# Optimization experiments

Hardware: AMD Instinct MI355X
Metric: run time of the kernel (lower is better)

Reference implementation:

```python
import jax, jax.numpy as jnp
import numpy as np

N_NODES = 50000
N_EDGES = 800000
N_GRAPHS = 256
IN_DIM = 128
HID = 512            # hidden_layer_size
H2 = HID // 2        # 256, conv channels
H4 = HID // 4        # 128


def _linear_init(key, fan_in, fan_out):
    kw, kb = jax.random.split(key)
    bound = 1.0 / np.sqrt(fan_in)
    W = jax.random.uniform(kw, (fan_in, fan_out), minval=-bound, maxval=bound, dtype=jnp.float32)
    b = jax.random.uniform(kb, (fan_out,), minval=-bound, maxval=bound, dtype=jnp.float32)
    return W, b


def setup_inputs() -> dict:
    key = jax.random.key(0)
    ks = jax.random.split(key, 8)
    x = jax.random.normal(ks[0], (N_NODES, IN_DIM), dtype=jnp.float32)
    edge_index = jax.random.randint(ks[1], (2, N_EDGES), 0, N_NODES, dtype=jnp.int64)
    batch = jnp.sort(jax.random.randint(ks[2], (N_NODES,), 0, N_GRAPHS, dtype=jnp.int64))
    W1, b1 = _linear_init(ks[3], IN_DIM, HID)
    Wc1, bc1 = _linear_init(ks[4], HID, H2)
    Wc2, bc2 = _linear_init(ks[5], H2, H2)
    W2, b2 = _linear_init(ks[6], H2, H4)
    W3, b3 = _linear_init(ks[7], H4, 1)
    return {"x": x, "edge_index": edge_index, "batch": batch,
            "W1": W1, "b1": b1, "Wc1": Wc1, "bc1": bc1,
            "Wc2": Wc2, "bc2": bc2, "W2": W2, "b2": b2, "W3": W3, "b3": b3}


def _gcn_conv(h, W, b, src, dst, norm):
    # PyG GCNConv: out = scatter_add(norm * (h @ W)[src] -> dst) + b
    hw = h @ W                                   # [N, C_out]
    msg = norm[:, None] * hw[src]                # [E+N, C_out] gather
    agg = jax.ops.segment_sum(msg, dst, num_segments=N_NODES)  # scatter-add
    return agg + b


def reference(x, edge_index, batch, W1, b1, Wc1, bc1, Wc2, bc2, W2, b2, W3, b3):
    # --- symmetric GCN normalization with self-loops (shared by both convs) ---
    loop = jnp.arange(N_NODES, dtype=edge_index.dtype)
    src = jnp.concatenate([edge_index[0], loop])
    dst = jnp.concatenate([edge_index[1], loop])
    deg = jax.ops.segment_sum(jnp.ones_like(dst, dtype=jnp.float32), dst, num_segments=N_NODES)
    dinv = jax.lax.rsqrt(deg)                    # deg >= 1 thanks to self-loops
    norm = dinv[src] * dinv[dst]                 # [E+N]

    h = jax.nn.relu(x @ W1 + b1)                 # lin1
    h = jax.nn.relu(_gcn_conv(h, Wc1, bc1, src, dst, norm))   # conv1
    h = jax.nn.relu(_gcn_conv(h, Wc2, bc2, src, dst, norm))   # conv2

    # global_mean_pool over graph ids
    sums = jax.ops.segment_sum(h, batch, num_segments=N_GRAPHS)
    counts = jax.ops.segment_sum(jnp.ones((N_NODES,), jnp.float32), batch, num_segments=N_GRAPHS)
    g = sums / jnp.maximum(counts, 1.0)[:, None]

    # F.dropout is identity in deterministic/eval reference
    g = jax.nn.relu(g @ W2 + b2)                 # lin2
    return g @ W3 + b3                           # lin3 -> [N_GRAPHS, 1]
```

## Files before the change

kernel.cpp:

```cpp
#include <hip/hip_runtime.h>
#include <hip/hip_bf16.h>

#define NN 50000
#define NE 800000
#define NG 256
#define DIN 128
#define DH 512
#define DC 256
#define DL 128
#define NB 49

#define XBF_OFF   0UL
#define H1BF_OFF  12800000UL
#define HWBF_OFF  64000000UL
#define H2BF_OFF  89600000UL
#define H3BF_OFF  115200000UL
#define W1T_OFF   140800000UL
#define WC1T_OFF  140931072UL
#define WC2T_OFF  141193216UL
#define CNT_OFF   141324288UL
#define FILL_OFF  141524288UL
#define DINV_OFF  141724288UL
#define RP_OFF    141924288UL
#define BSUM_OFF  142124416UL
#define EW_OFF    142124800UL

using bf16x8 = __attribute__((ext_vector_type(8))) short;
using u16x8  = __attribute__((ext_vector_type(8))) unsigned short;
using f32x4  = __attribute__((ext_vector_type(4))) float;

__device__ __forceinline__ short f2bf(float f) {
  unsigned u = __builtin_bit_cast(unsigned, f);
  unsigned r = u + 0x7fffu + ((u >> 16) & 1u);
  return (short)(r >> 16);
}
__device__ __forceinline__ float bf2f(unsigned short u) {
  return __builtin_bit_cast(float, (unsigned)u << 16);
}

__device__ __forceinline__ void gload_lds16(const void* g, void* l) {
  typedef const __attribute__((address_space(1))) unsigned gu32;
  typedef __attribute__((address_space(3))) unsigned lu32;
  __builtin_amdgcn_global_load_lds((gu32*)g, (lu32*)l, 16, 0, 0);
}

__global__ void count_in(const int* __restrict__ dst, int* __restrict__ cnt) {
  int e = blockIdx.x * blockDim.x + threadIdx.x;
  if (e < NE) atomicAdd(&cnt[dst[e]], 1);
}

__global__ __launch_bounds__(1024) void scan_p1(const int* __restrict__ cnt,
                                                int* __restrict__ rowptr,
                                                int* __restrict__ bsum,
                                                float* __restrict__ dinv) {
  __shared__ int wsum[16];
  const int idx = blockIdx.x * 1024 + threadIdx.x;
  const int lane = threadIdx.x & 63, wid = threadIdx.x >> 6;
  int v = (idx < NN) ? cnt[idx] : 0;
  int incl = v;
  #pragma unroll
  for (int s = 1; s < 64; s <<= 1) {
    int t = __shfl_up(incl, s, 64);
    if (lane >= s) incl += t;
  }
  if (lane == 63) wsum[wid] = incl;
  __syncthreads();
  if (wid == 0 && lane < 16) {
    int w = wsum[lane];
    int wincl = w;
    #pragma unroll
    for (int s = 1; s < 16; s <<= 1) {
      int t = __shfl_up(wincl, s, 64);
      if (lane >= s) wincl += t;
    }
    wsum[lane] = wincl - w;
    if (lane == 15) bsum[blockIdx.x] = wincl;
  }
  __syncthreads();
  if (idx < NN) {
    rowptr[idx] = wsum[wid] + incl - v;
    dinv[idx] = 1.0f / sqrtf((float)(v + 1));
  }
}

__global__ void scan_p2(int* __restrict__ bsum, int* __restrict__ rowptr) {
  const int lane = threadIdx.x;
  int v = (lane < NB) ? bsum[lane] : 0;
  int incl = v;
  #pragma unroll
  for (int s = 1; s < 64; s <<= 1) {
    int t = __shfl_up(incl, s, 64);
    if (lane >= s) incl += t;
  }
  if (lane < NB) bsum[lane] = incl - v;
  if (lane == 63) rowptr[NN] = incl;
}

__global__ __launch_bounds__(1024) void scan_p3(int* __restrict__ rowptr,
                                                const int* __restrict__ bsum) {
  const int idx = blockIdx.x * 1024 + threadIdx.x;
  if (idx < NN && blockIdx.x > 0) rowptr[idx] += bsum[blockIdx.x];
}

__global__ void fill_csr(const int* __restrict__ src, const int* __restrict__ dst,
                         const int* __restrict__ rowptr, int* __restrict__ fill,
                         const float* __restrict__ dinv, int2* __restrict__ ew) {
  int e = blockIdx.x * blockDim.x + threadIdx.x;
  if (e < NE) {
    int d = dst[e];
    int s = src[e];
    int pos = rowptr[d] + atomicAdd(&fill[d], 1);
    ew[pos] = make_int2(s, __float_as_int(dinv[d] * dinv[s]));
  }
}

__global__ void cvt_bf16(const float* __restrict__ in, short* __restrict__ out, int n8) {
  int i = blockIdx.x * blockDim.x + threadIdx.x;
  if (i >= n8) return;
  const float4* p = (const float4*)in + (long)i * 2;
  float4 a = p[0], b = p[1];
  bf16x8 o;
  o[0] = f2bf(a.x); o[1] = f2bf(a.y); o[2] = f2bf(a.z); o[3] = f2bf(a.w);
  o[4] = f2bf(b.x); o[5] = f2bf(b.y); o[6] = f2bf(b.z); o[7] = f2bf(b.w);
  *(bf16x8*)(out + (long)i * 8) = o;
}

__global__ void transpose_bf16(const float* __restrict__ in, short* __restrict__ out,
                               int K, int N) {
  int idx = blockIdx.x * blockDim.x + threadIdx.x;
  if (idx >= K * N) return;
  int n = idx / K, k = idx % K;
  out[idx] = f2bf(in[k * N + n]);
}

template<int DO_RELU, int HAS_BIAS>
__global__ __launch_bounds__(256) void gemm_mfma2(
    const short* __restrict__ A,
    const short* __restrict__ Bt,
    const float* __restrict__ bias,
    short* __restrict__ Cout, int M, int K, int N)
{
  __shared__ __align__(16) short As[128][32];
  __shared__ __align__(16) short Bs[128][32];
  const int tid  = threadIdx.x;
  const int lane = tid & 63;
  const int wave = tid >> 6;
  const int wr   = wave >> 1;
  const int wc   = wave & 1;
  const int bm = blockIdx.y * 128;
  const int bn = blockIdx.x * 128;

  const int srow = lane >> 2;
  const int scol = (lane & 3) * 8;

  f32x4 acc[4][4];
  #pragma unroll
  for (int m = 0; m < 4; ++m)
    #pragma unroll
    for (int n = 0; n < 4; ++n)
      acc[m][n] = f32x4{0.f, 0.f, 0.f, 0.f};

  const int fr = lane & 15;
  const int kb = (lane >> 4) * 8;

  for (int k0 = 0; k0 < K; k0 += 32) {
    #pragma unroll
    for (int j = 0; j < 2; ++j) {
      const int r = wave * 32 + j * 16;
      gload_lds16(A  + (long)(bm + r + srow) * K + k0 + scol, &As[r][0]);
      gload_lds16(Bt + (long)(bn + r + srow) * K + k0 + scol, &Bs[r][0]);
    }
    __syncthreads();
    bf16x8 af[4], bfr[4];
    #pragma unroll
    for (int m = 0; m < 4; ++m)
      af[m] = *(const bf16x8*)&As[wr * 64 + m * 16 + fr][kb];
    #pragma unroll
    for (int n = 0; n < 4; ++n)
      bfr[n] = *(const bf16x8*)&Bs[wc * 64 + n * 16 + fr][kb];
    #pragma unroll
    for (int m = 0; m < 4; ++m)
      #pragma unroll
      for (int n = 0; n < 4; ++n)
        acc[m][n] = __builtin_amdgcn_mfma_f32_16x16x32_bf16(af[m], bfr[n], acc[m][n], 0, 0, 0);
    __syncthreads();
  }

  const int cr4 = (lane >> 4) * 4;
  const int cc  = lane & 15;
  #pragma unroll
  for (int m = 0; m < 4; ++m) {
    #pragma unroll
    for (int r = 0; r < 4; ++r) {
      int gm = bm + wr * 64 + m * 16 + cr4 + r;
      if (gm >= M) continue;
      #pragma unroll
      for (int n = 0; n < 4; ++n) {
        int gn = bn + wc * 64 + n * 16 + cc;
        float v = acc[m][n][r];
        if (HAS_BIAS) v += bias[gn];
        if (DO_RELU) v = fmaxf(v, 0.f);
        Cout[(long)gm * N + gn] = f2bf(v);
      }
    }
  }
}

__global__ __launch_bounds__(256) void aggregate_v4(
    const unsigned short* __restrict__ hw, const int2* __restrict__ ew,
    const int* __restrict__ rowptr, const float* __restrict__ dinv,
    const float* __restrict__ bias, unsigned short* __restrict__ out)
{
  const int wid  = threadIdx.x >> 6;
  const int lane = threadIdx.x & 63;
  const int i = blockIdx.x * 4 + wid;
  if (i >= NN) return;
  const int half = lane >> 5;
  const int c0 = (lane & 31) * 8;

  float acc[8] = {0.f, 0.f, 0.f, 0.f, 0.f, 0.f, 0.f, 0.f};
  if (half == 0) {
    const float di = dinv[i];
    const float w = di * di;
    u16x8 sv = *(const u16x8*)(hw + (long)i * DC + c0);
    #pragma unroll
    for (int k = 0; k < 8; ++k) acc[k] = w * bf2f(sv[k]);
  }

  const int s0 = rowptr[i], s1 = rowptr[i + 1];
  int e = s0;
  for (; e + 16 <= s1; e += 16) {
    int nn[8]; float wv[8]; u16x8 vv[8];
    #pragma unroll
    for (int j = 0; j < 8; ++j) {
      int2 p = ew[e + 2 * j + half];
      nn[j] = p.x; wv[j] = __int_as_float(p.y);
    }
    #pragma unroll
    for (int j = 0; j < 8; ++j)
      vv[j] = *(const u16x8*)(hw + (long)nn[j] * DC + c0);
    #pragma unroll
    for (int j = 0; j < 8; ++j)
      #pragma unroll
      for (int k = 0; k < 8; ++k) acc[k] += wv[j] * bf2f(vv[j][k]);
  }
  for (; e + 2 <= s1; e += 2) {
    int2 p = ew[e + half];
    u16x8 v = *(const u16x8*)(hw + (long)p.x * DC + c0);
    float w = __int_as_float(p.y);
    #pragma unroll
    for (int k = 0; k < 8; ++k) acc[k] += w * bf2f(v[k]);
  }
  if (e < s1 && half == 0) {
    int2 p = ew[e];
    u16x8 v = *(const u16x8*)(hw + (long)p.x * DC + c0);
    float w = __int_as_float(p.y);
    #pragma unroll
    for (int k = 0; k < 8; ++k) acc[k] += w * bf2f(v[k]);
  }

  #pragma unroll
  for (int k = 0; k < 8; ++k) acc[k] += __shfl_xor(acc[k], 32, 64);

  if (half == 0) {
    u16x8 o;
    #pragma unroll
    for (int k = 0; k < 8; ++k) {
      float v = fmaxf(acc[k] + bias[c0 + k], 0.f);
      o[k] = (unsigned short)f2bf(v);
    }
    *(u16x8*)(out + (long)i * DC + c0) = o;
  }
}

__global__ __launch_bounds__(256) void pool_mlp_v3(
    const unsigned short* __restrict__ h, const int* __restrict__ batch,
    const float* __restrict__ W2, const float* __restrict__ b2,
    const float* __restrict__ W3, const float* __restrict__ b3,
    float* __restrict__ out)
{
  __shared__ float part[4][DC];
  __shared__ float gmean[DC];
  __shared__ float red[DL];
  const int g = blockIdx.x;
  const int t = threadIdx.x;
  const int wid = t >> 6;
  const int lane = t & 63;
  const int c0 = lane * 4;

  int lo = 0, hi = NN;
  while (lo < hi) { int mid = (lo + hi) >> 1; if (batch[mid] < g) lo = mid + 1; else hi = mid; }
  const int start = lo;
  hi = NN;
  while (lo < hi) { int mid = (lo + hi) >> 1; if (batch[mid] < g + 1) lo = mid + 1; else hi = mid; }
  const int end = lo;

  float4 a0 = {0.f, 0.f, 0.f, 0.f}, a1 = {0.f, 0.f, 0.f, 0.f};
  int i = start + wid;
  for (; i + 4 < end; i += 8) {
    ushort4 v0 = *(const ushort4*)(h + (long)i * DC + c0);
    ushort4 v1 = *(const ushort4*)(h + (long)(i + 4) * DC + c0);
    a0.x += bf2f(v0.x); a0.y += bf2f(v0.y); a0.z += bf2f(v0.z); a0.w += bf2f(v0.w);
    a1.x += bf2f(v1.x); a1.y += bf2f(v1.y); a1.z += bf2f(v1.z); a1.w += bf2f(v1.w);
  }
  if (i < end) {
    ushort4 v0 = *(const ushort4*)(h + (long)i * DC + c0);
    a0.x += bf2f(v0.x); a0.y += bf2f(v0.y); a0.z += bf2f(v0.z); a0.w += bf2f(v0.w);
  }
  a0.x += a1.x; a0.y += a1.y; a0.z += a1.z; a0.w += a1.w;
  *(float4*)&part[wid][c0] = a0;
  __syncthreads();
  if (wid == 0) {
    const float inv = 1.0f / fmaxf((float)(end - start), 1.f);
    float4 s0 = *(const float4*)&part[0][c0];
    float4 s1 = *(const float4*)&part[1][c0];
    float4 s2 = *(const float4*)&part[2][c0];
    float4 s3 = *(const float4*)&part[3][c0];
    float4 m;
    m.x = (s0.x + s1.x + s2.x + s3.x) * inv;
    m.y = (s0.y + s1.y + s2.y + s3.y) * inv;
    m.z = (s0.z + s1.z + s2.z + s3.z) * inv;
    m.w = (s0.w + s1.w + s2.w + s3.w) * inv;
    *(float4*)&gmean[c0] = m;
  }
  __syncthreads();
  if (t < DL) {
    float acc = b2[t];
    for (int k = 0; k < DC; ++k) acc = fmaf(gmean[k], W2[k * DL + t], acc);
    red[t] = fmaxf(acc, 0.f) * W3[t];
  }
  __syncthreads();
  for (int s2 = 64; s2 > 0; s2 >>= 1) {
    if (t < s2) red[t] += red[t + s2];
    __syncthreads();
  }
  if (t == 0) out[g] = red[0] + b3[0];
}

extern "C" void kernel_launch(void* const* d_in, const int* in_sizes, int n_in,
                              void* d_out, int out_size, void* d_ws, size_t ws_size,
                              hipStream_t stream) {
  const float* x    = (const float*)d_in[0];
  const int*   ei   = (const int*)d_in[1];
  const int*   bat  = (const int*)d_in[2];
  const float* W1   = (const float*)d_in[3];
  const float* b1   = (const float*)d_in[4];
  const float* Wc1  = (const float*)d_in[5];
  const float* bc1  = (const float*)d_in[6];
  const float* Wc2  = (const float*)d_in[7];
  const float* bc2  = (const float*)d_in[8];
  const float* W2   = (const float*)d_in[9];
  const float* b2   = (const float*)d_in[10];
  const float* W3   = (const float*)d_in[11];
  const float* b3   = (const float*)d_in[12];
  float* out = (float*)d_out;

  char* ws = (char*)d_ws;
  short* xbf    = (short*)(ws + XBF_OFF);
  short* h1bf   = (short*)(ws + H1BF_OFF);
  unsigned short* hwbf = (unsigned short*)(ws + HWBF_OFF);
  unsigned short* h2bf = (unsigned short*)(ws + H2BF_OFF);
  unsigned short* h3bf = (unsigned short*)(ws + H3BF_OFF);
  short* W1t    = (short*)(ws + W1T_OFF);
  short* Wc1t   = (short*)(ws + WC1T_OFF);
  short* Wc2t   = (short*)(ws + WC2T_OFF);
  int*   cnt    = (int*)  (ws + CNT_OFF);
  int*   fill   = (int*)  (ws + FILL_OFF);
  float* dinv   = (float*)(ws + DINV_OFF);
  int*   rowptr = (int*)  (ws + RP_OFF);
  int*   bsum   = (int*)  (ws + BSUM_OFF);
  int2*  ew     = (int2*) (ws + EW_OFF);

  const int* srcE = ei;
  const int* dstE = ei + NE;

  hipMemsetAsync(cnt, 0, 2 * NN * sizeof(int), stream);

  count_in<<<(NE + 255) / 256, 256, 0, stream>>>(dstE, cnt);
  scan_p1<<<NB, 1024, 0, stream>>>(cnt, rowptr, bsum, dinv);
  scan_p2<<<1, 64, 0, stream>>>(bsum, rowptr);
  scan_p3<<<NB, 1024, 0, stream>>>(rowptr, bsum);
  fill_csr<<<(NE + 255) / 256, 256, 0, stream>>>(srcE, dstE, rowptr, fill, dinv, ew);

  cvt_bf16<<<(NN * DIN / 8 + 255) / 256, 256, 0, stream>>>(x, xbf, NN * DIN / 8);
  transpose_bf16<<<(DIN * DH + 255) / 256, 256, 0, stream>>>(W1, W1t, DIN, DH);
  transpose_bf16<<<(DH * DC + 255) / 256, 256, 0, stream>>>(Wc1, Wc1t, DH, DC);
  transpose_bf16<<<(DC * DC + 255) / 256, 256, 0, stream>>>(Wc2, Wc2t, DC, DC);

  {
    dim3 grid(DH / 128, (NN + 127) / 128);
    gemm_mfma2<1, 1><<<grid, 256, 0, stream>>>(xbf, W1t, b1, h1bf, NN, DIN, DH);
  }
  {
    dim3 grid(DC / 128, (NN + 127) / 128);
    gemm_mfma2<0, 0><<<grid, 256, 0, stream>>>(h1bf, Wc1t, nullptr, (short*)hwbf, NN, DH, DC);
  }
  aggregate_v4<<<(NN + 3) / 4, 256, 0, stream>>>(hwbf, ew, rowptr, dinv, bc1, h2bf);
  {
    dim3 grid(DC / 128, (NN + 127) / 128);
    gemm_mfma2<0, 0><<<grid, 256, 0, stream>>>((const short*)h2bf, Wc2t, nullptr, (short*)hwbf, NN, DC, DC);
  }
  aggregate_v4<<<(NN + 3) / 4, 256, 0, stream>>>(hwbf, ew, rowptr, dinv, bc2, h3bf);

  pool_mlp_v3<<<NG, 256, 0, stream>>>(h3bf, bat, W2, b2, W3, b3, out);
}
```

Measured before the change: 364.0 us.

## Pack CSR edges into 32-bit words and split aggregation across column slices

```diff
diff --git a/kernel.cpp b/kernel.cpp
--- a/kernel.cpp
+++ b/kernel.cpp
@@ -9,6 +9,7 @@
 #define DC 256
 #define DL 128
 #define NB 49
+#define NSLICE 8
 
 #define XBF_OFF   0UL
 #define H1BF_OFF  12800000UL
@@ -104,13 +105,14 @@
 
 __global__ void fill_csr(const int* __restrict__ src, const int* __restrict__ dst,
                          const int* __restrict__ rowptr, int* __restrict__ fill,
-                         const float* __restrict__ dinv, int2* __restrict__ ew) {
+                         const float* __restrict__ dinv, unsigned* __restrict__ ewp) {
   int e = blockIdx.x * blockDim.x + threadIdx.x;
   if (e < NE) {
     int d = dst[e];
     int s = src[e];
     int pos = rowptr[d] + atomicAdd(&fill[d], 1);
-    ew[pos] = make_int2(s, __float_as_int(dinv[d] * dinv[s]));
+    float w = dinv[d] * dinv[s];
+    ewp[pos] = (unsigned)s | ((unsigned)(unsigned short)f2bf(w) << 16);
   }
 }
 
@@ -206,70 +208,53 @@
   }
 }
 
-__global__ __launch_bounds__(256) void aggregate_v4(
-    const unsigned short* __restrict__ hw, const int2* __restrict__ ew,
+__global__ __launch_bounds__(256) void aggregate_v5(
+    const unsigned short* __restrict__ hw, const unsigned* __restrict__ ewp,
     const int* __restrict__ rowptr, const float* __restrict__ dinv,
     const float* __restrict__ bias, unsigned short* __restrict__ out)
 {
-  const int wid  = threadIdx.x >> 6;
-  const int lane = threadIdx.x & 63;
-  const int i = blockIdx.x * 4 + wid;
+  const int slice = blockIdx.x & 7;
+  const int wid   = threadIdx.x >> 6;
+  const int lane  = threadIdx.x & 63;
+  const int i = (blockIdx.x >> 3) * 4 + wid;
   if (i >= NN) return;
-  const int half = lane >> 5;
-  const int c0 = (lane & 31) * 8;
-
-  float acc[8] = {0.f, 0.f, 0.f, 0.f, 0.f, 0.f, 0.f, 0.f};
-  if (half == 0) {
+  const int g = lane >> 3;
+  const int p = lane & 7;
+  const int c = slice * 32 + p * 4;
+
+  float a0 = 0.f, a1 = 0.f, a2 = 0.f, a3 = 0.f;
+  const int s0 = rowptr[i], s1 = rowptr[i + 1];
+  for (int e = s0; e < s1; e += 8) {
+    int ee = e + g;
+    unsigned pk = (ee < s1) ? __builtin_nontemporal_load(ewp + ee) : 0u;
+    int s = (int)(pk & 0xffffu);
+    float w = bf2f((unsigned short)(pk >> 16));
+    ushort4 v = *(const ushort4*)(hw + (long)s * DC + c);
+    a0 += w * bf2f(v.x); a1 += w * bf2f(v.y);
+    a2 += w * bf2f(v.z); a3 += w * bf2f(v.w);
+  }
+  if (g == 0) {
     const float di = dinv[i];
     const float w = di * di;
-    u16x8 sv = *(const u16x8*)(hw + (long)i * DC + c0);
-    #pragma unroll
-    for (int k = 0; k < 8; ++k) acc[k] = w * bf2f(sv[k]);
-  }
-
-  const int s0 = rowptr[i], s1 = rowptr[i + 1];
-  int e = s0;
-  for (; e + 16 <= s1; e += 16) {
-    int nn[8]; float wv[8]; u16x8 vv[8];
-    #pragma unroll
-    for (int j = 0; j < 8; ++j) {
-      int2 p = ew[e + 2 * j + half];
-      nn[j] = p.x; wv[j] = __int_as_float(p.y);
-    }
-    #pragma unroll
-    for (int j = 0; j < 8; ++j)
-      vv[j] = *(const u16x8*)(hw + (long)nn[j] * DC + c0);
-    #pragma unroll
-    for (int j = 0; j < 8; ++j)
-      #pragma unroll
-      for (int k = 0; k < 8; ++k) acc[k] += wv[j] * bf2f(vv[j][k]);
-  }
-  for (; e + 2 <= s1; e += 2) {
-    int2 p = ew[e + half];
-    u16x8 v = *(const u16x8*)(hw + (long)p.x * DC + c0);
-    float w = __int_as_float(p.y);
-    #pragma unroll
-    for (int k = 0; k < 8; ++k) acc[k] += w * bf2f(v[k]);
-  }
-  if (e < s1 && half == 0) {
-    int2 p = ew[e];
-    u16x8 v = *(const u16x8*)(hw + (long)p.x * DC + c0);
-    float w = __int_as_float(p.y);
-    #pragma unroll
-    for (int k = 0; k < 8; ++k) acc[k] += w * bf2f(v[k]);
-  }
-
-  #pragma unroll
-  for (int k = 0; k < 8; ++k) acc[k] += __shfl_xor(acc[k], 32, 64);
-
-  if (half == 0) {
-    u16x8 o;
-    #pragma unroll
-    for (int k = 0; k < 8; ++k) {
-      float v = fmaxf(acc[k] + bias[c0 + k], 0.f);
-      o[k] = (unsigned short)f2bf(v);
-    }
-    *(u16x8*)(out + (long)i * DC + c0) = o;
+    ushort4 sv = *(const ushort4*)(hw + (long)i * DC + c);
+    a0 += w * bf2f(sv.x); a1 += w * bf2f(sv.y);
+    a2 += w * bf2f(sv.z); a3 += w * bf2f(sv.w);
+  }
+  #pragma unroll
+  for (int m = 8; m < 64; m <<= 1) {
+    a0 += __shfl_xor(a0, m, 64);
+    a1 += __shfl_xor(a1, m, 64);
+    a2 += __shfl_xor(a2, m, 64);
+    a3 += __shfl_xor(a3, m, 64);
+  }
+  if (g == 0) {
+    const float4 bv = *(const float4*)(bias + c);
+    ushort4 o;
+    o.x = (unsigned short)f2bf(fmaxf(a0 + bv.x, 0.f));
+    o.y = (unsigned short)f2bf(fmaxf(a1 + bv.y, 0.f));
+    o.z = (unsigned short)f2bf(fmaxf(a2 + bv.z, 0.f));
+    o.w = (unsigned short)f2bf(fmaxf(a3 + bv.w, 0.f));
+    *(ushort4*)(out + (long)i * DC + c) = o;
   }
 }
 
@@ -369,7 +354,7 @@
   float* dinv   = (float*)(ws + DINV_OFF);
   int*   rowptr = (int*)  (ws + RP_OFF);
   int*   bsum   = (int*)  (ws + BSUM_OFF);
-  int2*  ew     = (int2*) (ws + EW_OFF);
+  unsigned* ewp = (unsigned*)(ws + EW_OFF);
 
   const int* srcE = ei;
   const int* dstE = ei + NE;
@@ -380,7 +365,7 @@
   scan_p1<<<NB, 1024, 0, stream>>>(cnt, rowptr, bsum, dinv);
   scan_p2<<<1, 64, 0, stream>>>(bsum, rowptr);
   scan_p3<<<NB, 1024, 0, stream>>>(rowptr, bsum);
-  fill_csr<<<(NE + 255) / 256, 256, 0, stream>>>(srcE, dstE, rowptr, fill, dinv, ew);
+  fill_csr<<<(NE + 255) / 256, 256, 0, stream>>>(srcE, dstE, rowptr, fill, dinv, ewp);
 
   cvt_bf16<<<(NN * DIN / 8 + 255) / 256, 256, 0, stream>>>(x, xbf, NN * DIN / 8);
   transpose_bf16<<<(DIN * DH + 255) / 256, 256, 0, stream>>>(W1, W1t, DIN, DH);
@@ -395,12 +380,12 @@
     dim3 grid(DC / 128, (NN + 127) / 128);
     gemm_mfma2<0, 0><<<grid, 256, 0, stream>>>(h1bf, Wc1t, nullptr, (short*)hwbf, NN, DH, DC);
   }
-  aggregate_v4<<<(NN + 3) / 4, 256, 0, stream>>>(hwbf, ew, rowptr, dinv, bc1, h2bf);
+  aggregate_v5<<<NSLICE * ((NN + 3) / 4), 256, 0, stream>>>(hwbf, ewp, rowptr, dinv, bc1, h2bf);
   {
     dim3 grid(DC / 128, (NN + 127) / 128);
     gemm_mfma2<0, 0><<<grid, 256, 0, stream>>>((const short*)h2bf, Wc2t, nullptr, (short*)hwbf, NN, DC, DC);
   }
-  aggregate_v4<<<(NN + 3) / 4, 256, 0, stream>>>(hwbf, ew, rowptr, dinv, bc2, h3bf);
+  aggregate_v5<<<NSLICE * ((NN + 3) / 4), 256, 0, stream>>>(hwbf, ewp, rowptr, dinv, bc2, h3bf);
 
   pool_mlp_v3<<<NG, 256, 0, stream>>>(h3bf, bat, W2, b2, W3, b3, out);
 }
```

After: 620.0 us. +70.4%, slower.
